# Kernel optimization log

Hardware: AMD Instinct MI355X
Metric: run time of the kernel (lower is better)

Reference implementation:

```python
import jax, jax.numpy as jnp
import numpy as np

HEADS = 4

def _rope(Q, K):
    # Q, K: [B, T, H, F]; split last dim into 4 chunks of w = F // 4
    w = Q.shape[-1] // 4
    T = Q.shape[-3]
    Q1r, Q1i, Q2r, Q2i = jnp.split(Q, 4, axis=-1)
    K1r, K1i, K2r, K2i = jnp.split(K, 4, axis=-1)
    Pt = jnp.arange(T, dtype=Q.dtype).reshape(1, -1, 1, 1)
    Df = (2.0 ** (-jnp.arange(w, dtype=Q.dtype))).reshape(1, 1, 1, -1)
    U = Pt * Df / 16.0
    Ur, Ui = jnp.sin(U), jnp.cos(U)  # names match the original (sin first)
    rot = lambda r, i: (r * Ur - i * Ui, r * Ui + i * Ur)
    Q1r, Q1i = rot(Q1r, Q1i)
    Q2r, Q2i = rot(Q2r, Q2i)
    K1r, K1i = rot(K1r, K1i)
    K2r, K2i = rot(K2r, K2i)
    return (jnp.concatenate([Q1r, Q1i], -1), jnp.concatenate([Q2r, Q2i], -1),
            jnp.concatenate([K1r, K1i], -1), jnp.concatenate([K2r, K2i], -1))


def setup_inputs() -> dict:
    key = jax.random.key(0)
    ks = jax.random.split(key, 8)
    B, F, T = 4, 512, 2048
    sd = 1.0 / np.sqrt(F)
    return {
        "x": jax.random.normal(ks[0], (B, F, T), jnp.float32),
        "Wq": jax.random.normal(ks[1], (F, F), jnp.float32) * sd,
        "bq": jax.random.normal(ks[2], (F,), jnp.float32) * sd,
        "Wk": jax.random.normal(ks[3], (F, F), jnp.float32) * sd,
        "bk": jax.random.normal(ks[4], (F,), jnp.float32) * sd,
        "Wv": jax.random.normal(ks[5], (F, F), jnp.float32) * sd,
        "bv": jax.random.normal(ks[6], (F,), jnp.float32) * sd,
        "s2": jax.random.uniform(ks[7], (HEADS,), jnp.float32),
    }


def reference(x, Wq, bq, Wk, bk, Wv, bv, s2):
    # x: [B, feat, T] -> transpose to [B, T, feat]; cond defaults to x
    B, F, T = x.shape
    H = HEADS
    hf = F // H
    scale = jnp.asarray(np.sqrt(F // 2), x.dtype)
    xt = jnp.swapaxes(x, -1, -2)  # [B, T, F]
    Q = (xt @ Wq.T + bq).reshape(B, T, H, hf)
    K = (xt @ Wk.T + bk).reshape(B, T, H, hf)
    V = (xt @ Wv.T + bv).reshape(B, T, H, hf)
    Q1, Q2, K1, K2 = _rope(Q, K)
    A1 = jax.nn.softmax(jnp.einsum('bqhf,bkhf->bhqk', Q1, K1) / scale, axis=-1)
    A2 = jax.nn.softmax(jnp.einsum('bqhf,bkhf->bhqk', Q2, K2) / scale, axis=-1)
    A = A1 - A2 * s2[None, :, None, None]
    R = jnp.einsum('bhqk,bkhf->bqhf', A, V)
    y = R.reshape(B, T, F)
    return jnp.swapaxes(xt + y, -1, -2)  # [B, feat, T]
```

## Files before the change

### kernel.cpp

```cpp
#include <hip/hip_runtime.h>
#include <math.h>

#define B_DIM 4
#define F_DIM 512
#define T_DIM 2048
#define H_DIM 4
#define HF    128

typedef __attribute__((ext_vector_type(8))) short short8;
typedef __attribute__((ext_vector_type(4))) float floatx4;

__device__ __forceinline__ unsigned short f2bf(float f) {
    return (unsigned short)((__float_as_uint(f) + 0x8000u) >> 16);
}

__device__ __forceinline__ unsigned pkbf2(float a, float b) {
    const unsigned ua = __float_as_uint(a) + 0x8000u;
    const unsigned ub = __float_as_uint(b) + 0x8000u;
    return __builtin_amdgcn_perm(ub, ua, 0x07060302u);
}

__device__ __forceinline__ short8 pack8(const float* v) {
    union { unsigned u[4]; short8 s; } r;
    #pragma unroll
    for (int j = 0; j < 4; ++j) r.u[j] = pkbf2(v[2*j], v[2*j+1]);
    return r.s;
}

__global__ __launch_bounds__(256)
void prep_kernel(const float* __restrict__ x,
                 const float* __restrict__ Wq, const float* __restrict__ Wk,
                 const float* __restrict__ Wv,
                 unsigned short* __restrict__ xt,
                 unsigned short* __restrict__ Wqb, unsigned short* __restrict__ Wkb,
                 unsigned short* __restrict__ Wvb)
{
    const int tid = threadIdx.x;
    if (blockIdx.z < B_DIM) {
        const int b  = blockIdx.z;
        const int t0 = blockIdx.x * 64;
        const int f0 = blockIdx.y * 64;
        __shared__ float Ls[64][67];
        const float* __restrict__ xb = x + (size_t)b * F_DIM * T_DIM;
        #pragma unroll
        for (int it = 0; it < 4; ++it) {
            const int fr = (tid >> 4) + 16 * it;
            const int tc = (tid & 15) << 2;
            const float4 v = *(const float4*)(xb + (size_t)(f0 + fr) * T_DIM + t0 + tc);
            Ls[fr][tc+0] = v.x; Ls[fr][tc+1] = v.y; Ls[fr][tc+2] = v.z; Ls[fr][tc+3] = v.w;
        }
        __syncthreads();
        const int f8 = tid & 7;
        const int tb = tid >> 3;
        #pragma unroll
        for (int it2 = 0; it2 < 2; ++it2) {
            const int t = tb + 32 * it2;
            float v[8];
            #pragma unroll
            for (int j = 0; j < 8; ++j) v[j] = Ls[8*f8 + j][t];
            *(short8*)(xt + ((size_t)b * T_DIM + t0 + t) * F_DIM + f0 + 8*f8) = pack8(v);
        }
    } else {
        const int blockId = blockIdx.y * 32 + blockIdx.x;
        const int g0 = blockId * 256 + tid;
        const int perW = F_DIM * F_DIM / 8;
        for (int chunk = g0; chunk < 3 * perW; chunk += 65536) {
            const int wsel = chunk / perW;
            const int rem  = chunk - wsel * perW;
            const float* __restrict__ Ws = (wsel == 0) ? Wq : (wsel == 1) ? Wk : Wv;
            unsigned short* __restrict__ Wd = (wsel == 0) ? Wqb : (wsel == 1) ? Wkb : Wvb;
            float v[8];
            *(float4*)&v[0] = *(const float4*)(Ws + (size_t)rem * 8);
            *(float4*)&v[4] = *(const float4*)(Ws + (size_t)rem * 8 + 4);
            *(short8*)(Wd + (size_t)rem * 8) = pack8(v);
        }
    }
}

#define ASTR 136

__global__ __launch_bounds__(256, 3)
void proj_kernel(const unsigned short* __restrict__ xt,
                 const unsigned short* __restrict__ Wqb,
                 const unsigned short* __restrict__ Wkb,
                 const unsigned short* __restrict__ Wvb,
                 const float* __restrict__ bq, const float* __restrict__ bk,
                 const float* __restrict__ bv,
                 unsigned short* __restrict__ Qb, unsigned short* __restrict__ Kb,
                 unsigned short* __restrict__ Vtb)
{
    __shared__ unsigned short As[128][ASTR];
    __shared__ unsigned short Bs[64][ASTR];

    const int tid  = threadIdx.x;
    const int w    = tid >> 6;
    const int lane = tid & 63;
    const int ln15 = lane & 15;
    const int quad = lane >> 4;

    const bool is_v = (blockIdx.z >= 8);
    int t0, fo0, b;
    const unsigned short *Asrc, *Bsrc;
    if (!is_v) {
        t0  = blockIdx.x * 128;
        fo0 = blockIdx.y * 64;
        b   = blockIdx.z >> 1;
        Asrc = xt + (size_t)b * T_DIM * F_DIM + (size_t)t0 * F_DIM;
        Bsrc = ((blockIdx.z & 1) ? Wkb : Wqb) + (size_t)fo0 * F_DIM;
    } else {
        const int idx = blockIdx.y * 16 + blockIdx.x;
        fo0 = (idx >> 5) * 128;
        t0  = (idx & 31) * 64;
        b   = blockIdx.z - 8;
        Asrc = Wvb + (size_t)fo0 * F_DIM;
        Bsrc = xt + (size_t)b * T_DIM * F_DIM + (size_t)t0 * F_DIM;
    }

    floatx4 acc[2][4];
    #pragma unroll
    for (int mi = 0; mi < 2; ++mi)
        #pragma unroll
        for (int nt = 0; nt < 4; ++nt) acc[mi][nt] = (floatx4){0.f,0.f,0.f,0.f};

    for (int f0 = 0; f0 < F_DIM; f0 += 128) {
        __syncthreads();
        #pragma unroll
        for (int it = 0; it < 8; ++it) {
            const int idx = tid + it * 256;
            const int r = idx >> 4, c = (idx & 15) * 8;
            *(short8*)&As[r][c] = *(const short8*)(Asrc + (size_t)r * F_DIM + f0 + c);
        }
        #pragma unroll
        for (int it = 0; it < 4; ++it) {
            const int idx = tid + it * 256;
            const int r = idx >> 4, c = (idx & 15) * 8;
            *(short8*)&Bs[r][c] = *(const short8*)(Bsrc + (size_t)r * F_DIM + f0 + c);
        }
        __syncthreads();
        #pragma unroll
        for (int ks = 0; ks < 4; ++ks) {
            short8 a[2], bb[4];
            a[0] = *(const short8*)&As[w*32      + ln15][ks*32 + quad*8];
            a[1] = *(const short8*)&As[w*32 + 16 + ln15][ks*32 + quad*8];
            #pragma unroll
            for (int nt = 0; nt < 4; ++nt)
                bb[nt] = *(const short8*)&Bs[16*nt + ln15][ks*32 + quad*8];
            #pragma unroll
            for (int mi = 0; mi < 2; ++mi)
                #pragma unroll
                for (int nt = 0; nt < 4; ++nt)
                    acc[mi][nt] = __builtin_amdgcn_mfma_f32_16x16x32_bf16(
                        a[mi], bb[nt], acc[mi][nt], 0, 0, 0);
        }
    }

    if (!is_v) {
        const int which = blockIdx.z & 1;
        const float* bias = which ? bk : bq;
        unsigned short* __restrict__ Out =
            (which ? Kb : Qb) + (size_t)b * T_DIM * F_DIM;
        const float oscale = which ? 1.0f : 0.0625f * 1.4426950408889634f;
        float bn[4];
        #pragma unroll
        for (int nt = 0; nt < 4; ++nt) bn[nt] = bias[fo0 + 16*nt + ln15];
        const float pw[2] = {
            __uint_as_float((unsigned)(123 - ln15) << 23),
            __uint_as_float((unsigned)(107 - ln15) << 23)
        };
        #pragma unroll
        for (int mi = 0; mi < 2; ++mi) {
            #pragma unroll
            for (int r = 0; r < 4; ++r) {
                const int t = t0 + w*32 + 16*mi + quad*4 + r;
                unsigned short* rowp = Out + (size_t)t * F_DIM + fo0;
                #pragma unroll
                for (int pr = 0; pr < 2; ++pr) {
                    const int wi = 16*pr + ln15;
                    const float re = acc[mi][pr  ][r] + bn[pr];
                    const float im = acc[mi][pr+2][r] + bn[pr+2];
                    const float u = (float)t * pw[pr];
                    float sn, cs;
                    __sincosf(u, &sn, &cs);
                    rowp[wi]      = f2bf((re * sn - im * cs) * oscale);
                    rowp[wi + 32] = f2bf((re * cs + im * sn) * oscale);
                }
            }
        }
    } else {
        #pragma unroll
        for (int mi = 0; mi < 2; ++mi) {
            #pragma unroll
            for (int r = 0; r < 4; ++r) {
                const int fo = fo0 + w*32 + 16*mi + quad*4 + r;
                const float bvv = bv[fo];
                unsigned short* rowp = Vtb + ((size_t)b * F_DIM + fo) * T_DIM + t0;
                #pragma unroll
                for (int nt = 0; nt < 4; ++nt)
                    rowp[16*nt + ln15] = f2bf(acc[mi][nt][r] + bvv);
            }
        }
    }
}

__global__ __launch_bounds__(512, 2)
void attn_kernel(const unsigned short* __restrict__ Qb,
                 const unsigned short* __restrict__ Kb,
                 const unsigned short* __restrict__ Vtb,
                 const float* __restrict__ x,
                 const float* __restrict__ s2g,
                 float* __restrict__ out)
{
    __shared__ unsigned short smem[2][16384];

    const int tid  = threadIdx.x;
    const int w8   = tid >> 6;
    const int half = w8 >> 2;
    const int w    = w8 & 3;
    const int lane = tid & 63;
    const int ln15 = lane & 15;
    const int quad = lane >> 4;
    const int t256 = tid & 255;

    const int q0 = blockIdx.x * 64;
    const int h  = blockIdx.y;
    const int b  = blockIdx.z;
    const int kbase = half << 10;

    unsigned short* __restrict__ Ks = &smem[half][0];
    unsigned short* __restrict__ Vs = &smem[half][8192];

    const unsigned short* __restrict__ Qg =
        Qb + ((size_t)b * T_DIM + q0 + w * 16) * F_DIM + h * HF;
    const unsigned short* __restrict__ Kg =
        Kb + (size_t)b * T_DIM * F_DIM + h * HF;
    const unsigned short* __restrict__ Vg =
        Vtb + ((size_t)b * F_DIM + h * HF) * T_DIM;

    short8 qa[4];
    #pragma unroll
    for (int c = 0; c < 4; ++c)
        qa[c] = *(const short8*)(Qg + (size_t)ln15 * F_DIM + quad * 8 + 32 * c);

    floatx4 O1t[8], O2t[8];
    #pragma unroll
    for (int ft = 0; ft < 8; ++ft) {
        O1t[ft] = (floatx4){0.f, 0.f, 0.f, 0.f};
        O2t[ft] = (floatx4){0.f, 0.f, 0.f, 0.f};
    }
    float l1 = 0.f, l2 = 0.f;

    short8 kpre[4], vpre[4];
    #pragma unroll
    for (int it = 0; it < 4; ++it) {
        const int idx = t256 + it * 256;
        kpre[it] = *(const short8*)(Kg + (size_t)(kbase + (idx >> 4)) * F_DIM + (idx & 15) * 8);
    }
    #pragma unroll
    for (int it = 0; it < 4; ++it) {
        const int idx = t256 + it * 256;
        vpre[it] = *(const short8*)(Vg + (size_t)(idx >> 3) * T_DIM + kbase + (idx & 7) * 8);
    }

    for (int k0 = 0; k0 < 1024; k0 += 64) {
        __syncthreads();
        #pragma unroll
        for (int it = 0; it < 4; ++it) {
            const int idx = t256 + it * 256;
            const int r = idx >> 4, c = idx & 15;
            const int rp = (r & 32) | ((r & 4) << 2) | ((r & 24) >> 1) | (r & 3);
            *(short8*)&Ks[rp * 128 + (c ^ (rp & 15)) * 8] = kpre[it];
        }
        #pragma unroll
        for (int it = 0; it < 4; ++it) {
            const int idx = t256 + it * 256;
            const int r = idx >> 3, c = idx & 7;
            *(short8*)&Vs[r * 64 + (c ^ (r & 7)) * 8] = vpre[it];
        }
        __syncthreads();

        if (k0 + 64 < 1024) {
            #pragma unroll
            for (int it = 0; it < 4; ++it) {
                const int idx = t256 + it * 256;
                kpre[it] = *(const short8*)(Kg + (size_t)(kbase + k0 + 64 + (idx >> 4)) * F_DIM + (idx & 15) * 8);
            }
            #pragma unroll
            for (int it = 0; it < 4; ++it) {
                const int idx = t256 + it * 256;
                vpre[it] = *(const short8*)(Vg + (size_t)(idx >> 3) * T_DIM + kbase + k0 + 64 + (idx & 7) * 8);
            }
        }

        floatx4 S1t[4], S2t[4];
        #pragma unroll
        for (int t = 0; t < 4; ++t) {
            const unsigned short* krow = &Ks[(16 * t + ln15) * 128];
            const short8 k0f = *(const short8*)(krow + ((quad     ) ^ ln15) * 8);
            const short8 k1f = *(const short8*)(krow + ((quad +  4) ^ ln15) * 8);
            const short8 k2f = *(const short8*)(krow + ((quad +  8) ^ ln15) * 8);
            const short8 k3f = *(const short8*)(krow + ((quad + 12) ^ ln15) * 8);
            floatx4 z = (floatx4){0.f, 0.f, 0.f, 0.f};
            floatx4 s = __builtin_amdgcn_mfma_f32_16x16x32_bf16(k0f, qa[0], z, 0, 0, 0);
            S1t[t]    = __builtin_amdgcn_mfma_f32_16x16x32_bf16(k1f, qa[1], s, 0, 0, 0);
            floatx4 u = __builtin_amdgcn_mfma_f32_16x16x32_bf16(k2f, qa[2], z, 0, 0, 0);
            S2t[t]    = __builtin_amdgcn_mfma_f32_16x16x32_bf16(k3f, qa[3], u, 0, 0, 0);
        }

        float e1[16], e2[16];
        #pragma unroll
        for (int t = 0; t < 4; ++t)
            #pragma unroll
            for (int r = 0; r < 4; ++r) {
                e1[4*t + r] = __builtin_amdgcn_exp2f(S1t[t][r]);
                e2[4*t + r] = __builtin_amdgcn_exp2f(S2t[t][r]);
            }
        #pragma unroll
        for (int i = 0; i < 16; ++i) { l1 += e1[i]; l2 += e2[i]; }

        short8 p1f[2], p2f[2];
        p1f[0] = pack8(&e1[0]);  p1f[1] = pack8(&e1[8]);
        p2f[0] = pack8(&e2[0]);  p2f[1] = pack8(&e2[8]);

        #pragma unroll
        for (int p = 0; p < 2; ++p) {
            #pragma unroll
            for (int ft = 0; ft < 8; ++ft) {
                const short8 va = *(const short8*)
                    (&Vs[(16*ft + ln15) * 64 + (((4*p + quad) ^ (ln15 & 7))) * 8]);
                O1t[ft] = __builtin_amdgcn_mfma_f32_16x16x32_bf16(va, p1f[p], O1t[ft], 0, 0, 0);
                O2t[ft] = __builtin_amdgcn_mfma_f32_16x16x32_bf16(va, p2f[p], O2t[ft], 0, 0, 0);
            }
        }
    }

    l1 += __shfl_xor(l1, 16); l1 += __shfl_xor(l1, 32);
    l2 += __shfl_xor(l2, 16); l2 += __shfl_xor(l2, 32);

    float* comb = (float*)&smem[0][0];
    __syncthreads();
    if (half == 1) {
        if (quad == 0) { comb[w*16 + ln15] = l1; comb[64 + w*16 + ln15] = l2; }
        #pragma unroll
        for (int ft = 0; ft < 8; ++ft)
            #pragma unroll
            for (int r = 0; r < 4; ++r)
                comb[128 + (ft*4 + r) * 256 + w*64 + lane] = O1t[ft][r];
    }
    __syncthreads();
    if (half == 0) {
        l1 += comb[w*16 + ln15];
        l2 += comb[64 + w*16 + ln15];
        #pragma unroll
        for (int ft = 0; ft < 8; ++ft)
            #pragma unroll
            for (int r = 0; r < 4; ++r)
                O1t[ft][r] += comb[128 + (ft*4 + r) * 256 + w*64 + lane];
    }
    __syncthreads();
    if (half == 1) {
        #pragma unroll
        for (int ft = 0; ft < 8; ++ft)
            #pragma unroll
            for (int r = 0; r < 4; ++r)
                comb[128 + (ft*4 + r) * 256 + w*64 + lane] = O2t[ft][r];
    }
    __syncthreads();
    if (half == 0) {
        #pragma unroll
        for (int ft = 0; ft < 8; ++ft)
            #pragma unroll
            for (int r = 0; r < 4; ++r)
                O2t[ft][r] += comb[128 + (ft*4 + r) * 256 + w*64 + lane];

        const float s2h = s2g[h];
        const float i1 = 1.f / l1;
        const float i2 = s2h / l2;
        const size_t obase = (size_t)b * F_DIM * T_DIM;
        const int f0 = h * HF;
        const int t = q0 + w * 16 + ln15;
        #pragma unroll
        for (int ft = 0; ft < 8; ++ft) {
            #pragma unroll
            for (int r = 0; r < 4; ++r) {
                const int feat = 16*ft + 4*quad + r;
                const size_t idx = obase + (size_t)(f0 + feat) * T_DIM + t;
                out[idx] = x[idx] + O1t[ft][r] * i1 - O2t[ft][r] * i2;
            }
        }
    }
}

extern "C" void kernel_launch(void* const* d_in, const int* in_sizes, int n_in,
                              void* d_out, int out_size, void* d_ws, size_t ws_size,
                              hipStream_t stream)
{
    const float* x  = (const float*)d_in[0];
    const float* Wq = (const float*)d_in[1];
    const float* bq = (const float*)d_in[2];
    const float* Wk = (const float*)d_in[3];
    const float* bk = (const float*)d_in[4];
    const float* Wv = (const float*)d_in[5];
    const float* bv = (const float*)d_in[6];
    const float* s2 = (const float*)d_in[7];
    float* out = (float*)d_out;

    const size_t per = (size_t)B_DIM * T_DIM * F_DIM;
    const size_t wsz = (size_t)F_DIM * F_DIM;
    unsigned short* xt  = (unsigned short*)d_ws;
    unsigned short* Wqb = xt + per;
    unsigned short* Wkb = Wqb + wsz;
    unsigned short* Wvb = Wkb + wsz;
    unsigned short* Qb  = Wvb + wsz;
    unsigned short* Kb  = Qb + per;
    unsigned short* Vtb = Kb + per;

    hipLaunchKernelGGL(prep_kernel, dim3(32, 8, 5), dim3(256), 0, stream,
                       x, Wq, Wk, Wv, xt, Wqb, Wkb, Wvb);

    hipLaunchKernelGGL(proj_kernel, dim3(16, 8, 12), dim3(256), 0, stream,
                       xt, Wqb, Wkb, Wvb, bq, bk, bv, Qb, Kb, Vtb);

    hipLaunchKernelGGL(attn_kernel, dim3(32, 4, 4), dim3(512), 0, stream,
                       Qb, Kb, Vtb, x, s2, out);
}
```

Measured before the change: 104.6 us.

## Double query tile per wave, stage K/V via direct global-to-LDS loads

Each wave now handles two 16-query groups, so a block covers 128 queries and every K/V fragment read from LDS feeds twice as many MFMAs. K and V tiles are copied straight from global memory into double-buffered LDS with global_load_lds, replacing the register prefetch and LDS store pass. Block indices are also swizzled to change the order blocks visit the data. In exchange the accumulator register footprint doubles while launch bounds still request two blocks per CU, and LDS use grows to 128KB, which risks register spills and halves the grid.

```diff
diff --git a/kernel.cpp b/kernel.cpp
--- a/kernel.cpp
+++ b/kernel.cpp
@@ -25,6 +25,12 @@
     #pragma unroll
     for (int j = 0; j < 4; ++j) r.u[j] = pkbf2(v[2*j], v[2*j+1]);
     return r.s;
+}
+
+__device__ __forceinline__ void gload16(const unsigned short* g, unsigned short* l) {
+    __builtin_amdgcn_global_load_lds(
+        (const __attribute__((address_space(1))) void*)g,
+        (__attribute__((address_space(3))) void*)l, 16, 0, 0);
 }
 
 __global__ __launch_bounds__(256)
@@ -210,116 +216,122 @@
                  const float* __restrict__ s2g,
                  float* __restrict__ out)
 {
-    __shared__ unsigned short smem[2][16384];
+    __shared__ unsigned short smem[2][2][16384];
 
     const int tid  = threadIdx.x;
     const int w8   = tid >> 6;
     const int half = w8 >> 2;
-    const int w    = w8 & 3;
+    const int qg   = w8 & 3;
     const int lane = tid & 63;
     const int ln15 = lane & 15;
     const int quad = lane >> 4;
-    const int t256 = tid & 255;
-
-    const int q0 = blockIdx.x * 64;
-    const int h  = blockIdx.y;
-    const int b  = blockIdx.z;
+
+    const int flat = blockIdx.x + 16 * (blockIdx.y + 4 * blockIdx.z);
+    const int swz  = (flat & 7) * 32 + (flat >> 3);
+    const int q0 = (swz & 15) * 128;
+    const int h  = (swz >> 4) & 3;
+    const int b  = swz >> 6;
+
     const int kbase = half << 10;
 
-    unsigned short* __restrict__ Ks = &smem[half][0];
-    unsigned short* __restrict__ Vs = &smem[half][8192];
-
     const unsigned short* __restrict__ Qg =
-        Qb + ((size_t)b * T_DIM + q0 + w * 16) * F_DIM + h * HF;
+        Qb + ((size_t)b * T_DIM + q0 + qg * 32) * F_DIM + h * HF;
     const unsigned short* __restrict__ Kg =
         Kb + (size_t)b * T_DIM * F_DIM + h * HF;
     const unsigned short* __restrict__ Vg =
         Vtb + ((size_t)b * F_DIM + h * HF) * T_DIM;
 
-    short8 qa[4];
-    #pragma unroll
-    for (int c = 0; c < 4; ++c)
-        qa[c] = *(const short8*)(Qg + (size_t)ln15 * F_DIM + quad * 8 + 32 * c);
-
-    floatx4 O1t[8], O2t[8];
-    #pragma unroll
-    for (int ft = 0; ft < 8; ++ft) {
-        O1t[ft] = (floatx4){0.f, 0.f, 0.f, 0.f};
-        O2t[ft] = (floatx4){0.f, 0.f, 0.f, 0.f};
-    }
-    float l1 = 0.f, l2 = 0.f;
-
-    short8 kpre[4], vpre[4];
+    int koff[4], voff[4];
     #pragma unroll
     for (int it = 0; it < 4; ++it) {
-        const int idx = t256 + it * 256;
-        kpre[it] = *(const short8*)(Kg + (size_t)(kbase + (idx >> 4)) * F_DIM + (idx & 15) * 8);
-    }
-    #pragma unroll
-    for (int it = 0; it < 4; ++it) {
-        const int idx = t256 + it * 256;
-        vpre[it] = *(const short8*)(Vg + (size_t)(idx >> 3) * T_DIM + kbase + (idx & 7) * 8);
-    }
+        const int m = qg * 4 + it;
+        {
+            const int rd = 4 * m + (lane >> 4);
+            const int r  = (rd & 32) | ((rd & 12) << 1) | ((rd & 16) >> 2) | (rd & 3);
+            const int c  = (lane & 15) ^ (rd & 15);
+            koff[it] = r * F_DIM + c * 8;
+        }
+        {
+            const int rd = 8 * m + (lane >> 3);
+            const int c  = (lane & 7) ^ (rd & 7);
+            voff[it] = rd * T_DIM + c * 8;
+        }
+    }
+
+    auto stage = [&](int buf, int k) {
+        unsigned short* Kd = &smem[half][buf][0]    + qg * 2048;
+        unsigned short* Vd = &smem[half][buf][8192] + qg * 2048;
+        const unsigned short* Kp = Kg + (size_t)(kbase + k) * F_DIM;
+        const unsigned short* Vp = Vg + (kbase + k);
+        #pragma unroll
+        for (int it = 0; it < 4; ++it) {
+            gload16(Kp + koff[it], Kd + it * 512);
+            gload16(Vp + voff[it], Vd + it * 512);
+        }
+    };
+
+    short8 qa[2][4];
+    #pragma unroll
+    for (int g = 0; g < 2; ++g)
+        #pragma unroll
+        for (int c = 0; c < 4; ++c)
+            qa[g][c] = *(const short8*)(Qg + (size_t)(g * 16 + ln15) * F_DIM + quad * 8 + 32 * c);
+
+    floatx4 O1t[2][8], O2t[2][8];
+    #pragma unroll
+    for (int g = 0; g < 2; ++g)
+        #pragma unroll
+        for (int ft = 0; ft < 8; ++ft) {
+            O1t[g][ft] = (floatx4){0.f, 0.f, 0.f, 0.f};
+            O2t[g][ft] = (floatx4){0.f, 0.f, 0.f, 0.f};
+        }
+    float l1[2] = {0.f, 0.f}, l2[2] = {0.f, 0.f};
+
+    stage(0, 0);
 
     for (int k0 = 0; k0 < 1024; k0 += 64) {
+        asm volatile("s_waitcnt vmcnt(0)" ::: "memory");
         __syncthreads();
-        #pragma unroll
-        for (int it = 0; it < 4; ++it) {
-            const int idx = t256 + it * 256;
-            const int r = idx >> 4, c = idx & 15;
-            const int rp = (r & 32) | ((r & 4) << 2) | ((r & 24) >> 1) | (r & 3);
-            *(short8*)&Ks[rp * 128 + (c ^ (rp & 15)) * 8] = kpre[it];
-        }
-        #pragma unroll
-        for (int it = 0; it < 4; ++it) {
-            const int idx = t256 + it * 256;
-            const int r = idx >> 3, c = idx & 7;
-            *(short8*)&Vs[r * 64 + (c ^ (r & 7)) * 8] = vpre[it];
-        }
-        __syncthreads();
-
-        if (k0 + 64 < 1024) {
-            #pragma unroll
-            for (int it = 0; it < 4; ++it) {
-                const int idx = t256 + it * 256;
-                kpre[it] = *(const short8*)(Kg + (size_t)(kbase + k0 + 64 + (idx >> 4)) * F_DIM + (idx & 15) * 8);
-            }
-            #pragma unroll
-            for (int it = 0; it < 4; ++it) {
-                const int idx = t256 + it * 256;
-                vpre[it] = *(const short8*)(Vg + (size_t)(idx >> 3) * T_DIM + kbase + k0 + 64 + (idx & 7) * 8);
-            }
-        }
-
-        floatx4 S1t[4], S2t[4];
-        #pragma unroll
-        for (int t = 0; t < 4; ++t) {
-            const unsigned short* krow = &Ks[(16 * t + ln15) * 128];
-            const short8 k0f = *(const short8*)(krow + ((quad     ) ^ ln15) * 8);
-            const short8 k1f = *(const short8*)(krow + ((quad +  4) ^ ln15) * 8);
-            const short8 k2f = *(const short8*)(krow + ((quad +  8) ^ ln15) * 8);
-            const short8 k3f = *(const short8*)(krow + ((quad + 12) ^ ln15) * 8);
-            floatx4 z = (floatx4){0.f, 0.f, 0.f, 0.f};
-            floatx4 s = __builtin_amdgcn_mfma_f32_16x16x32_bf16(k0f, qa[0], z, 0, 0, 0);
-            S1t[t]    = __builtin_amdgcn_mfma_f32_16x16x32_bf16(k1f, qa[1], s, 0, 0, 0);
-            floatx4 u = __builtin_amdgcn_mfma_f32_16x16x32_bf16(k2f, qa[2], z, 0, 0, 0);
-            S2t[t]    = __builtin_amdgcn_mfma_f32_16x16x32_bf16(k3f, qa[3], u, 0, 0, 0);
-        }
-
-        float e1[16], e2[16];
-        #pragma unroll
-        for (int t = 0; t < 4; ++t)
-            #pragma unroll
-            for (int r = 0; r < 4; ++r) {
-                e1[4*t + r] = __builtin_amdgcn_exp2f(S1t[t][r]);
-                e2[4*t + r] = __builtin_amdgcn_exp2f(S2t[t][r]);
-            }
-        #pragma unroll
-        for (int i = 0; i < 16; ++i) { l1 += e1[i]; l2 += e2[i]; }
-
-        short8 p1f[2], p2f[2];
-        p1f[0] = pack8(&e1[0]);  p1f[1] = pack8(&e1[8]);
-        p2f[0] = pack8(&e2[0]);  p2f[1] = pack8(&e2[8]);
+        const int buf = (k0 >> 6) & 1;
+        if (k0 + 64 < 1024) stage(buf ^ 1, k0 + 64);
+
+        const unsigned short* Ks = &smem[half][buf][0];
+        const unsigned short* Vs = &smem[half][buf][8192];
+
+        short8 p1f[2][2], p2f[2][2];
+        #pragma unroll
+        for (int tp = 0; tp < 2; ++tp) {
+            float e1[2][8], e2[2][8];
+            #pragma unroll
+            for (int tt = 0; tt < 2; ++tt) {
+                const int t = tp * 2 + tt;
+                const unsigned short* krow = &Ks[(16 * t + ln15) * 128];
+                const short8 k0f = *(const short8*)(krow + ((quad     ) ^ ln15) * 8);
+                const short8 k1f = *(const short8*)(krow + ((quad +  4) ^ ln15) * 8);
+                const short8 k2f = *(const short8*)(krow + ((quad +  8) ^ ln15) * 8);
+                const short8 k3f = *(const short8*)(krow + ((quad + 12) ^ ln15) * 8);
+                #pragma unroll
+                for (int g = 0; g < 2; ++g) {
+                    floatx4 z = (floatx4){0.f, 0.f, 0.f, 0.f};
+                    floatx4 s = __builtin_amdgcn_mfma_f32_16x16x32_bf16(k0f, qa[g][0], z, 0, 0, 0);
+                    s         = __builtin_amdgcn_mfma_f32_16x16x32_bf16(k1f, qa[g][1], s, 0, 0, 0);
+                    floatx4 u = __builtin_amdgcn_mfma_f32_16x16x32_bf16(k2f, qa[g][2], z, 0, 0, 0);
+                    u         = __builtin_amdgcn_mfma_f32_16x16x32_bf16(k3f, qa[g][3], u, 0, 0, 0);
+                    #pragma unroll
+                    for (int r = 0; r < 4; ++r) {
+                        e1[g][tt*4 + r] = __builtin_amdgcn_exp2f(s[r]);
+                        e2[g][tt*4 + r] = __builtin_amdgcn_exp2f(u[r]);
+                    }
+                }
+            }
+            #pragma unroll
+            for (int g = 0; g < 2; ++g) {
+                #pragma unroll
+                for (int j = 0; j < 8; ++j) { l1[g] += e1[g][j]; l2[g] += e2[g][j]; }
+                p1f[g][tp] = pack8(&e1[g][0]);
+                p2f[g][tp] = pack8(&e2[g][0]);
+            }
+        }
 
         #pragma unroll
         for (int p = 0; p < 2; ++p) {
@@ -327,64 +339,90 @@
             for (int ft = 0; ft < 8; ++ft) {
                 const short8 va = *(const short8*)
                     (&Vs[(16*ft + ln15) * 64 + (((4*p + quad) ^ (ln15 & 7))) * 8]);
-                O1t[ft] = __builtin_amdgcn_mfma_f32_16x16x32_bf16(va, p1f[p], O1t[ft], 0, 0, 0);
-                O2t[ft] = __builtin_amdgcn_mfma_f32_16x16x32_bf16(va, p2f[p], O2t[ft], 0, 0, 0);
-            }
-        }
-    }
-
-    l1 += __shfl_xor(l1, 16); l1 += __shfl_xor(l1, 32);
-    l2 += __shfl_xor(l2, 16); l2 += __shfl_xor(l2, 32);
-
-    float* comb = (float*)&smem[0][0];
+                O1t[0][ft] = __builtin_amdgcn_mfma_f32_16x16x32_bf16(va, p1f[0][p], O1t[0][ft], 0, 0, 0);
+                O1t[1][ft] = __builtin_amdgcn_mfma_f32_16x16x32_bf16(va, p1f[1][p], O1t[1][ft], 0, 0, 0);
+                O2t[0][ft] = __builtin_amdgcn_mfma_f32_16x16x32_bf16(va, p2f[0][p], O2t[0][ft], 0, 0, 0);
+                O2t[1][ft] = __builtin_amdgcn_mfma_f32_16x16x32_bf16(va, p2f[1][p], O2t[1][ft], 0, 0, 0);
+            }
+        }
+    }
+
+    #pragma unroll
+    for (int g = 0; g < 2; ++g) {
+        l1[g] += __shfl_xor(l1[g], 16); l1[g] += __shfl_xor(l1[g], 32);
+        l2[g] += __shfl_xor(l2[g], 16); l2[g] += __shfl_xor(l2[g], 32);
+    }
+
+    float* comb = (float*)&smem[0][0][0];
     __syncthreads();
     if (half == 1) {
-        if (quad == 0) { comb[w*16 + ln15] = l1; comb[64 + w*16 + ln15] = l2; }
-        #pragma unroll
-        for (int ft = 0; ft < 8; ++ft)
-            #pragma unroll
-            for (int r = 0; r < 4; ++r)
-                comb[128 + (ft*4 + r) * 256 + w*64 + lane] = O1t[ft][r];
+        if (quad == 0) {
+            #pragma unroll
+            for (int g = 0; g < 2; ++g) {
+                comb[      qg*32 + g*16 + ln15] = l1[g];
+                comb[128 + qg*32 + g*16 + ln15] = l2[g];
+            }
+        }
+        #pragma unroll
+        for (int g = 0; g < 2; ++g)
+            #pragma unroll
+            for (int ft = 0; ft < 8; ++ft)
+                #pragma unroll
+                for (int r = 0; r < 4; ++r)
+                    comb[512 + (((g*8 + ft)*4 + r) * 256) + qg*64 + lane] = O1t[g][ft][r];
     }
     __syncthreads();
     if (half == 0) {
-        l1 += comb[w*16 + ln15];
-        l2 += comb[64 + w*16 + ln15];
-        #pragma unroll
-        for (int ft = 0; ft < 8; ++ft)
-            #pragma unroll
-            for (int r = 0; r < 4; ++r)
-                O1t[ft][r] += comb[128 + (ft*4 + r) * 256 + w*64 + lane];
+        #pragma unroll
+        for (int g = 0; g < 2; ++g) {
+            l1[g] += comb[      qg*32 + g*16 + ln15];
+            l2[g] += comb[128 + qg*32 + g*16 + ln15];
+        }
+        #pragma unroll
+        for (int g = 0; g < 2; ++g)
+            #pragma unroll
+            for (int ft = 0; ft < 8; ++ft)
+                #pragma unroll
+                for (int r = 0; r < 4; ++r)
+                    O1t[g][ft][r] += comb[512 + (((g*8 + ft)*4 + r) * 256) + qg*64 + lane];
     }
     __syncthreads();
     if (half == 1) {
         #pragma unroll
-        for (int ft = 0; ft < 8; ++ft)
-            #pragma unroll
-            for (int r = 0; r < 4; ++r)
-                comb[128 + (ft*4 + r) * 256 + w*64 + lane] = O2t[ft][r];
+        for (int g = 0; g < 2; ++g)
+            #pragma unroll
+            for (int ft = 0; ft < 8; ++ft)
+                #pragma unroll
+                for (int r = 0; r < 4; ++r)
+                    comb[512 + (((g*8 + ft)*4 + r) * 256) + qg*64 + lane] = O2t[g][ft][r];
     }
     __syncthreads();
     if (half == 0) {
         #pragma unroll
-        for (int ft = 0; ft < 8; ++ft)
-            #pragma unroll
-            for (int r = 0; r < 4; ++r)
-                O2t[ft][r] += comb[128 + (ft*4 + r) * 256 + w*64 + lane];
+        for (int g = 0; g < 2; ++g)
+            #pragma unroll
+            for (int ft = 0; ft < 8; ++ft)
+                #pragma unroll
+                for (int r = 0; r < 4; ++r)
+                    O2t[g][ft][r] += comb[512 + (((g*8 + ft)*4 + r) * 256) + qg*64 + lane];
 
         const float s2h = s2g[h];
-        const float i1 = 1.f / l1;
-        const float i2 = s2h / l2;
+        float i1[2], i2[2];
+        #pragma unroll
+        for (int g = 0; g < 2; ++g) { i1[g] = 1.f / l1[g]; i2[g] = s2h / l2[g]; }
         const size_t obase = (size_t)b * F_DIM * T_DIM;
         const int f0 = h * HF;
-        const int t = q0 + w * 16 + ln15;
-        #pragma unroll
-        for (int ft = 0; ft < 8; ++ft) {
-            #pragma unroll
-            for (int r = 0; r < 4; ++r) {
-                const int feat = 16*ft + 4*quad + r;
-                const size_t idx = obase + (size_t)(f0 + feat) * T_DIM + t;
-                out[idx] = x[idx] + O1t[ft][r] * i1 - O2t[ft][r] * i2;
+        #pragma unroll
+        for (int g = 0; g < 2; ++g) {
+            const int t = q0 + qg*32 + g*16 + ln15;
+            #pragma unroll
+            for (int ft = 0; ft < 8; ++ft) {
+                #pragma unroll
+                for (int r = 0; r < 4; ++r) {
+                    const int feat = 16*ft + 4*quad + r;
+                    const size_t idx = obase + (size_t)(f0 + feat) * T_DIM + t;
+                    out[idx] = x[idx] + O1t[g][ft][r] * i1[g] - O2t[g][ft][r] * i2[g];
+                }
             }
         }
     }
@@ -420,6 +458,6 @@
     hipLaunchKernelGGL(proj_kernel, dim3(16, 8, 12), dim3(256), 0, stream,
                        xt, Wqb, Wkb, Wvb, bq, bk, bv, Qb, Kb, Vtb);
 
-    hipLaunchKernelGGL(attn_kernel, dim3(32, 4, 4), dim3(512), 0, stream,
+    hipLaunchKernelGGL(attn_kernel, dim3(16, 4, 4), dim3(512), 0, stream,
                        Qb, Kb, Vtb, x, s2, out);
 }
```

New measurement: 93.31 us. 1.12x faster.
